# Kernel tuning notes

Hardware: AMD Instinct MI355X
Metric: run time of the kernel (lower is better)

Reference implementation:

```python
import jax, jax.numpy as jnp
import numpy as np

NUM_HEADS = 16
KV_CHANNELS = 128
MASK_FILL = -10000.0  # TE attention_mask_func fill value


def setup_inputs() -> dict:
    key = jax.random.key(0)
    k1, k2, k3 = jax.random.split(key, 3)
    S, B, H = 2048, 2, 2048
    hidden_states = jax.random.normal(k1, (S, B, H), dtype=jnp.float32)
    attention_mask = jnp.zeros((B, 1, S, S), dtype=bool)  # True = masked out
    qkv_weight = jax.random.normal(k2, (H, 3 * H), dtype=jnp.float32) * (1.0 / np.sqrt(H))
    qkv_bias = jnp.zeros((3 * H,), dtype=jnp.float32)
    proj_weight = jax.random.normal(k3, (H, H), dtype=jnp.float32) * (1.0 / np.sqrt(H))
    proj_bias = jnp.zeros((H,), dtype=jnp.float32)
    return {
        "hidden_states": hidden_states,
        "attention_mask": attention_mask,
        "qkv_weight": qkv_weight,
        "qkv_bias": qkv_bias,
        "proj_weight": proj_weight,
        "proj_bias": proj_bias,
    }


def reference(hidden_states, attention_mask, qkv_weight, qkv_bias, proj_weight, proj_bias):
    S, B, H = hidden_states.shape
    nh, d = NUM_HEADS, KV_CHANNELS
    # QKV GEMM: [s,b,H] @ [H,3H] -> [s,b,3H] -> [s,b,nh,3d] -> split
    mixed = hidden_states @ qkv_weight + qkv_bias
    mixed = mixed.reshape(S, B, nh, 3 * d)
    q, k, v = jnp.split(mixed, 3, axis=-1)  # each [s,b,nh,d]
    # BMM1 with 1/sqrt(d) scaling (layer_number=None -> no layer scaling)
    norm_factor = jnp.asarray(np.sqrt(d), dtype=hidden_states.dtype)
    scores = jnp.einsum("sbhd,tbhd->bhst", q, k) / norm_factor  # [b,nh,s,s]
    # causal mask (future positions masked) OR'd with provided bool padding mask
    causal = ~jnp.tril(jnp.ones((S, S), dtype=bool))  # True above diagonal
    mask = jnp.logical_or(causal[None, None], attention_mask)
    scores = jnp.where(mask, jnp.asarray(MASK_FILL, scores.dtype), scores)
    probs = jax.nn.softmax(scores, axis=-1)
    # dropout is identity in eval mode (training=False)
    # BMM2: [b,nh,s,t] x [t,b,nh,d] -> [s,b,nh,d] -> [s,b,H]
    context = jnp.einsum("bhst,tbhd->sbhd", probs, v).reshape(S, B, H)
    # output projection; TE Dense(use_bias=False, return_bias=True) returns bias
    out = context @ proj_weight
    return out, proj_bias
```

## Files before the change

### kernel.cpp

```cpp
#include <hip/hip_runtime.h>
#include <cstdint>
#include <math.h>

#define S_LEN 2048
#define BATCH 2
#define HID   2048
#define NHEAD 16
#define DHEAD 128

typedef _Float16 h8 __attribute__((ext_vector_type(8)));
typedef _Float16 h4 __attribute__((ext_vector_type(4)));
typedef float f32x4 __attribute__((ext_vector_type(4)));

__device__ __forceinline__ void gload16(const void* g, void* l) {
  __builtin_amdgcn_global_load_lds(
      (const __attribute__((address_space(1))) unsigned int*)g,
      (__attribute__((address_space(3))) unsigned int*)l, 16, 0, 0);
}

template <bool HAS_BIAS, bool OUT_HALF>
__global__ __launch_bounds__(512) void gemm_256v2(
    const _Float16* __restrict__ A, const _Float16* __restrict__ Bt,
    const float* __restrict__ bias, void* __restrict__ Cout, int M, int N,
    int K) {
  __shared__ _Float16 LA[2][16384];
  __shared__ _Float16 LB[2][16384];
  const int tid = (int)threadIdx.x;
  const int wave = tid >> 6, lane = tid & 63;
  const int ln = lane & 15, quad = lane >> 4;
  const int wm = wave >> 2, wn = wave & 3;
  const int bm = (int)blockIdx.y * 256, bn = (int)blockIdx.x * 256;
  const int NT = K >> 6;

  const int gc8 = ((lane & 7) ^ (lane >> 3)) * 8;
  const int rbase = wave * 8 + (lane >> 3);
  uint32_t oA[4], oB[4];
#pragma unroll
  for (int q = 0; q < 4; q++) {
    oA[q] = (uint32_t)(bm + q * 64 + rbase) * (uint32_t)K + (uint32_t)gc8;
    oB[q] = (uint32_t)(bn + q * 64 + rbase) * (uint32_t)K + (uint32_t)gc8;
  }

#define STAGEA(bb_, u_)                                                  \
  {                                                                      \
    _Pragma("unroll") for (int q = 0; q < 4; q++)                        \
        gload16(A + (oA[q] + (uint32_t)(u_)*64u),                        \
                &LA[bb_][q * 4096 + wave * 512]);                        \
  }
#define STAGEB(bb_, u_)                                                  \
  {                                                                      \
    _Pragma("unroll") for (int q = 0; q < 4; q++)                        \
        gload16(Bt + (oB[q] + (uint32_t)(u_)*64u),                       \
                &LB[bb_][q * 4096 + wave * 512]);                        \
  }

  const int arow = ln * 64;
  const int sc0 = ((quad ^ (ln & 7))) * 8;
  const int sc1 = (((4 + quad) ^ (ln & 7))) * 8;
  const int abase = wm * 8192;
  const int bbase = wn * 4096;

  f32x4 acc[8][4];
#pragma unroll
  for (int m = 0; m < 8; m++)
#pragma unroll
    for (int n = 0; n < 4; n++) acc[m][n] = (f32x4){0.f, 0.f, 0.f, 0.f};
  h8 aF[4][2], bF[4][2];

#define HALF(mo_)                                                            \
  _Pragma("unroll") for (int mm_ = 0; mm_ < 4; mm_++)                        \
      _Pragma("unroll") for (int nn_ = 0; nn_ < 4; nn_++) {                  \
    acc[(mo_) + mm_][nn_] = __builtin_amdgcn_mfma_f32_16x16x32_f16(          \
        aF[mm_][0], bF[nn_][0], acc[(mo_) + mm_][nn_], 0, 0, 0);             \
    acc[(mo_) + mm_][nn_] = __builtin_amdgcn_mfma_f32_16x16x32_f16(          \
        aF[mm_][1], bF[nn_][1], acc[(mo_) + mm_][nn_], 0, 0, 0);             \
  }

  STAGEA(0, 0) STAGEB(0, 0)
  STAGEA(1, 1) STAGEB(1, 1)
  asm volatile("s_waitcnt vmcnt(8)" ::: "memory");
  __builtin_amdgcn_s_barrier();

  for (int u = 0; u < NT; ++u) {
    const int bb = u & 1;

#pragma unroll
    for (int m = 0; m < 4; m++) {
      aF[m][0] = *(const h8*)&LA[bb][abase + m * 1024 + arow + sc0];
      aF[m][1] = *(const h8*)&LA[bb][abase + m * 1024 + arow + sc1];
    }
#pragma unroll
    for (int n = 0; n < 4; n++) {
      bF[n][0] = *(const h8*)&LB[bb][bbase + n * 1024 + arow + sc0];
      bF[n][1] = *(const h8*)&LB[bb][bbase + n * 1024 + arow + sc1];
    }
    __builtin_amdgcn_s_barrier();
    __builtin_amdgcn_s_setprio(1);
    HALF(0)
    __builtin_amdgcn_s_setprio(0);
    __builtin_amdgcn_s_barrier();

#pragma unroll
    for (int m = 0; m < 4; m++) {
      aF[m][0] = *(const h8*)&LA[bb][abase + (m + 4) * 1024 + arow + sc0];
      aF[m][1] = *(const h8*)&LA[bb][abase + (m + 4) * 1024 + arow + sc1];
    }
    if (u + 2 < NT) {
      STAGEA(bb, u + 2) STAGEB(bb, u + 2)
      asm volatile("s_waitcnt vmcnt(8)" ::: "memory");
    } else if (u + 1 < NT) {
      asm volatile("s_waitcnt vmcnt(0)" ::: "memory");
    }
    __builtin_amdgcn_s_barrier();
    __builtin_amdgcn_s_setprio(1);
    HALF(4)
    __builtin_amdgcn_s_setprio(0);
    __builtin_amdgcn_s_barrier();
  }
#undef HALF
#undef STAGEA
#undef STAGEB

#pragma unroll
  for (int m = 0; m < 8; m++) {
#pragma unroll
    for (int r = 0; r < 4; r++) {
      const size_t row = (size_t)(bm + wm * 128 + m * 16 + quad * 4 + r);
#pragma unroll
      for (int n = 0; n < 4; n++) {
        const int col = bn + wn * 64 + n * 16 + ln;
        float v = acc[m][n][r];
        if (HAS_BIAS) v += bias[col];
        if (OUT_HALF)
          ((_Float16*)Cout)[row * N + col] = (_Float16)v;
        else
          ((float*)Cout)[row * N + col] = v;
      }
    }
  }
}

template <bool HAS_BIAS, bool OUT_HALF>
__global__ __launch_bounds__(512) void gemm_128(
    const _Float16* __restrict__ A, const _Float16* __restrict__ Bt,
    const float* __restrict__ bias, void* __restrict__ Cout, int M, int N,
    int K) {
  __shared__ _Float16 LA[2][8192];
  __shared__ _Float16 LB[2][16384];
  const int tid = (int)threadIdx.x;
  const int wave = tid >> 6, lane = tid & 63;
  const int ln = lane & 15, quad = lane >> 4;
  const int wm = wave >> 2, wn = wave & 3;
  const int bm = (int)blockIdx.y * 128, bn = (int)blockIdx.x * 256;
  const int NT = K >> 6;

  const int gc8 = ((lane & 7) ^ (lane >> 3)) * 8;
  const uint32_t oA0 =
      (uint32_t)(bm + wave * 8 + (lane >> 3)) * (uint32_t)K + (uint32_t)gc8;
  const uint32_t oA1 = oA0 + (uint32_t)(64 * K);
  const uint32_t oB00 =
      (uint32_t)(bn + wave * 16 + (lane >> 3)) * (uint32_t)K + (uint32_t)gc8;
  const uint32_t oB01 = oB00 + (uint32_t)(8 * K);
  const uint32_t oB10 = oB00 + (uint32_t)(128 * K);
  const uint32_t oB11 = oB10 + (uint32_t)(8 * K);

#define STAGE128(bb_, u_)                                                    \
  {                                                                          \
    gload16(A + (oA0 + (uint32_t)(u_)*64u), &LA[bb_][wave * 512]);           \
    gload16(A + (oA1 + (uint32_t)(u_)*64u), &LA[bb_][4096 + wave * 512]);    \
    gload16(Bt + (oB00 + (uint32_t)(u_)*64u), &LB[bb_][wave * 1024]);        \
    gload16(Bt + (oB01 + (uint32_t)(u_)*64u), &LB[bb_][wave * 1024 + 512]);  \
    gload16(Bt + (oB10 + (uint32_t)(u_)*64u), &LB[bb_][8192 + wave * 1024]); \
    gload16(Bt + (oB11 + (uint32_t)(u_)*64u),                                \
            &LB[bb_][8192 + wave * 1024 + 512]);                             \
  }

  const int arow = ln * 64;
  const int sc0 = ((quad ^ (ln & 7))) * 8;
  const int sc1 = (((4 + quad) ^ (ln & 7))) * 8;
  const int abase = wm * 4096;
  const int bbase = wn * 4096;

  f32x4 acc[4][4];
#pragma unroll
  for (int m = 0; m < 4; m++)
#pragma unroll
    for (int n = 0; n < 4; n++) acc[m][n] = (f32x4){0.f, 0.f, 0.f, 0.f};
  h8 aF[4][2], bF[4][2];

#define HQUAD(n0_)                                                           \
  _Pragma("unroll") for (int mm_ = 0; mm_ < 4; mm_++)                        \
      _Pragma("unroll") for (int nn_ = 0; nn_ < 2; nn_++) {                  \
    acc[mm_][(n0_) + nn_] = __builtin_amdgcn_mfma_f32_16x16x32_f16(          \
        aF[mm_][0], bF[(n0_) + nn_][0], acc[mm_][(n0_) + nn_], 0, 0, 0);     \
    acc[mm_][(n0_) + nn_] = __builtin_amdgcn_mfma_f32_16x16x32_f16(          \
        aF[mm_][1], bF[(n0_) + nn_][1], acc[mm_][(n0_) + nn_], 0, 0, 0);     \
  }

  STAGE128(0, 0)
  STAGE128(1, 1)
  asm volatile("s_waitcnt vmcnt(6)" ::: "memory");
  __builtin_amdgcn_s_barrier();

  for (int u = 0; u < NT; ++u) {
    const int bb = u & 1;

#pragma unroll
    for (int m = 0; m < 4; m++) {
      aF[m][0] = *(const h8*)&LA[bb][abase + m * 1024 + arow + sc0];
      aF[m][1] = *(const h8*)&LA[bb][abase + m * 1024 + arow + sc1];
    }
#pragma unroll
    for (int n = 0; n < 2; n++) {
      bF[n][0] = *(const h8*)&LB[bb][bbase + n * 1024 + arow + sc0];
      bF[n][1] = *(const h8*)&LB[bb][bbase + n * 1024 + arow + sc1];
    }
    __builtin_amdgcn_s_barrier();
    __builtin_amdgcn_s_setprio(1);
    HQUAD(0)
    __builtin_amdgcn_s_setprio(0);
    __builtin_amdgcn_s_barrier();

#pragma unroll
    for (int n = 2; n < 4; n++) {
      bF[n][0] = *(const h8*)&LB[bb][bbase + n * 1024 + arow + sc0];
      bF[n][1] = *(const h8*)&LB[bb][bbase + n * 1024 + arow + sc1];
    }
    if (u + 2 < NT) {
      STAGE128(bb, u + 2)
      asm volatile("s_waitcnt vmcnt(6)" ::: "memory");
    } else if (u + 1 < NT) {
      asm volatile("s_waitcnt vmcnt(0)" ::: "memory");
    }
    __builtin_amdgcn_s_barrier();
    __builtin_amdgcn_s_setprio(1);
    HQUAD(2)
    __builtin_amdgcn_s_setprio(0);
    __builtin_amdgcn_s_barrier();
  }
#undef HQUAD
#undef STAGE128

#pragma unroll
  for (int m = 0; m < 4; m++) {
#pragma unroll
    for (int r = 0; r < 4; r++) {
      const size_t row = (size_t)(bm + wm * 64 + m * 16 + quad * 4 + r);
#pragma unroll
      for (int n = 0; n < 4; n++) {
        const int col = bn + wn * 64 + n * 16 + ln;
        float v = acc[m][n][r];
        if (HAS_BIAS) v += bias[col];
        if (OUT_HALF)
          ((_Float16*)Cout)[row * N + col] = (_Float16)v;
        else
          ((float*)Cout)[row * N + col] = v;
      }
    }
  }
}

__global__ __launch_bounds__(256) void transpose_cvt(
    const float* __restrict__ in, _Float16* __restrict__ out, int K, int N) {
  __shared__ float t[64][65];
  const int bn = blockIdx.x * 64, bk = blockIdx.y * 64;
  const int tid = (int)threadIdx.x;
  {
    const int r0 = tid >> 4, c4 = (tid & 15) * 4;
#pragma unroll
    for (int i = 0; i < 4; i++) {
      const int r = r0 + 16 * i;
      float4 v = *(const float4*)&in[(size_t)(bk + r) * N + bn + c4];
      t[r][c4] = v.x;
      t[r][c4 + 1] = v.y;
      t[r][c4 + 2] = v.z;
      t[r][c4 + 3] = v.w;
    }
  }
  __syncthreads();
  {
    const int c0 = tid >> 4, r4 = (tid & 15) * 4;
#pragma unroll
    for (int i = 0; i < 4; i++) {
      const int c = c0 + 16 * i;
      h4 o = {(_Float16)t[r4][c], (_Float16)t[r4 + 1][c],
              (_Float16)t[r4 + 2][c], (_Float16)t[r4 + 3][c]};
      *(h4*)&out[(size_t)(bn + c) * K + bk + r4] = o;
    }
  }
}

__global__ __launch_bounds__(256) void cvt_fp16(const float* __restrict__ in,
                                                _Float16* __restrict__ out,
                                                int n4) {
  int i = blockIdx.x * blockDim.x + threadIdx.x;
  if (i < n4) {
    float4 v = ((const float4*)in)[i];
    h4 o = {(_Float16)v.x, (_Float16)v.y, (_Float16)v.z, (_Float16)v.w};
    *(h4*)&out[4 * (size_t)i] = o;
  }
}

__global__ __launch_bounds__(256) void pack_mask(
    const unsigned char* __restrict__ m, uint32_t* __restrict__ pm) {
  const int i = blockIdx.x * 256 + threadIdx.x;
  const int w = i & 63, r = (i >> 6) & (S_LEN - 1), b = i >> 17;
  const uint32_t* src =
      (const uint32_t*)(m + ((size_t)b * S_LEN + r) * S_LEN + w * 32);
  uint32_t bits = 0;
#pragma unroll
  for (int k = 0; k < 8; k++) {
    const uint32_t v = src[k];
    bits |= ((v & 0x000000FFu) ? 1u : 0u) << (4 * k);
    bits |= ((v & 0x0000FF00u) ? 1u : 0u) << (4 * k + 1);
    bits |= ((v & 0x00FF0000u) ? 1u : 0u) << (4 * k + 2);
    bits |= ((v & 0xFF000000u) ? 1u : 0u) << (4 * k + 3);
  }
  const int c0 = w * 32;
  uint32_t caus;
  if (c0 > r) {
    caus = 0xFFFFFFFFu;
  } else if (r - c0 >= 31) {
    caus = 0u;
  } else {
    caus = ~((2u << (r - c0)) - 1u);
  }
  pm[i] = bits | caus;
}

__global__ __launch_bounds__(256) void pack_kv(
    const _Float16* __restrict__ mixed, _Float16* __restrict__ KP,
    _Float16* __restrict__ VP) {
  __shared__ _Float16 Tv[128 * 40];
  const int kt = blockIdx.x;
  const int z = blockIdx.y;
  const int kb = kt * 32;
  const int tid = threadIdx.x;
  const size_t RS = (size_t)BATCH * NHEAD * 384;
  const _Float16* base = mixed + (size_t)z * 384;

  {
    const int r = tid >> 3, d0 = (tid & 7) * 16;
    const _Float16* src = base + (size_t)(kb + r) * RS + 256 + d0;
    h8 v0 = *(const h8*)src;
    h8 v1 = *(const h8*)(src + 8);
#pragma unroll
    for (int e = 0; e < 8; e++) Tv[(d0 + e) * 40 + r] = v0[e];
#pragma unroll
    for (int e = 0; e < 8; e++) Tv[(d0 + 8 + e) * 40 + r] = v1[e];
  }
  __syncthreads();

  const size_t tb = ((size_t)z * 64 + kt) * 8 * 512;
#pragma unroll
  for (int c = 0; c < 2; c++) {
    const int idx = tid + 256 * c;
    const int i = idx >> 6, l = idx & 63;
    const int ln = l & 15, quad = l >> 4;
    {
      const int jn = i >> 2, kq = i & 3;
      h8 v = *(const h8*)(base + (size_t)(kb + 16 * jn + ln) * RS + 128 +
                          32 * kq + 8 * quad);
      *(h8*)&KP[tb + (size_t)i * 512 + l * 8] = v;
    }
    {
      h8 v = *(const h8*)&Tv[(16 * i + ln) * 40 + 8 * quad];
      *(h8*)&VP[tb + (size_t)i * 512 + l * 8] = v;
    }
  }
}

__global__ __launch_bounds__(512) void flash_attn_v9(
    const _Float16* __restrict__ mixed, const _Float16* __restrict__ KP,
    const _Float16* __restrict__ VP, const uint32_t* __restrict__ pmask,
    _Float16* __restrict__ ctx) {
  const int bid = (int)blockIdx.x;
  const int x = bid & 7, s = bid >> 3;
  const int z = x * 4 + (s & 3);
  const int qt = 15 - (s >> 2);
  const int h = z & (NHEAD - 1), b = z >> 4;
  const int qb = qt * 128;
  const int tid = threadIdx.x;
  const int wave = tid >> 6, lane = tid & 63;
  const int ln = lane & 15, quad = lane >> 4;

  __shared__ _Float16 Kbuf[2][8 * 512];
  __shared__ _Float16 Vbuf[2][8 * 512];
  __shared__ _Float16 St[8][16 * 40];

  const size_t RS = (size_t)BATCH * NHEAD * 384;
  const _Float16* base = mixed + (size_t)z * 384;
  const uint32_t* pmb = pmask + (size_t)b * S_LEN * 64;
  const float scale = 0.08838834764831845f;

  h8 qfrag[4];
  {
    const size_t row = (size_t)(qb + 16 * wave + ln);
#pragma unroll
    for (int kq = 0; kq < 4; kq++) {
      h8 v = *(const h8*)(base + row * RS + 32 * kq + 8 * quad);
#pragma unroll
      for (int j = 0; j < 8; j++) v[j] = (_Float16)((float)v[j] * scale);
      qfrag[kq] = v;
    }
  }

  f32x4 o[8];
#pragma unroll
  for (int nt = 0; nt < 8; nt++) o[nt] = (f32x4){0.f, 0.f, 0.f, 0.f};
  float lpart[4] = {0.f, 0.f, 0.f, 0.f};

  const int ntiles = 4 * qt + 4;

  const size_t zt = (size_t)z * 64;
#define STAGE(kt_, buf_)                                            \
  {                                                                 \
    const size_t tbk = (zt + (kt_)) * (8 * 512) + lane * 8;         \
    gload16(KP + tbk + wave * 512, &Kbuf[buf_][wave * 512]);        \
    gload16(VP + tbk + wave * 512, &Vbuf[buf_][wave * 512]);        \
  }

  STAGE(0, 0)

  const uint32_t* pmr = pmb + (size_t)(qb + 16 * wave + 4 * quad) * 64;

  for (int kt = 0; kt < ntiles; kt++) {
    const int cur = kt & 1;
    __syncthreads();

    if (kt + 1 < ntiles) STAGE(kt + 1, cur ^ 1)

    uint32_t mw[4];
#pragma unroll
    for (int r = 0; r < 4; r++) mw[r] = pmr[(size_t)r * 64 + kt];

    f32x4 sreg[2];
    sreg[0] = (f32x4){0.f, 0.f, 0.f, 0.f};
    sreg[1] = (f32x4){0.f, 0.f, 0.f, 0.f};
#pragma unroll
    for (int kq = 0; kq < 4; kq++) {
#pragma unroll
      for (int jn = 0; jn < 2; jn++) {
        h8 bk = *(const h8*)&Kbuf[cur][(jn * 4 + kq) * 512 + lane * 8];
        sreg[jn] = __builtin_amdgcn_mfma_f32_16x16x32_f16(qfrag[kq], bk,
                                                          sreg[jn], 0, 0, 0);
      }
    }

#pragma unroll
    for (int r = 0; r < 4; r++) {
      const uint32_t ms = mw[r] >> ln;
#pragma unroll
      for (int jn = 0; jn < 2; jn++) {
        const float sv =
            ((ms >> (16 * jn)) & 1u) ? -10000.0f : sreg[jn][r];
        const float p = __expf(sv);
        lpart[r] += p;
        St[wave][(4 * quad + r) * 40 + 16 * jn + ln] = (_Float16)p;
      }
    }
    __threadfence_block();

    {
      h8 ap = *(const h8*)&St[wave][ln * 40 + 8 * quad];
#pragma unroll
      for (int nt = 0; nt < 8; nt++) {
        h8 bv = *(const h8*)&Vbuf[cur][nt * 512 + lane * 8];
        o[nt] = __builtin_amdgcn_mfma_f32_16x16x32_f16(ap, bv, o[nt], 0, 0, 0);
      }
    }
  }
#undef STAGE

#pragma unroll
  for (int r = 0; r < 4; r++) {
    float l = lpart[r];
#pragma unroll
    for (int off = 8; off >= 1; off >>= 1) l += __shfl_xor(l, off, 16);
    const float inv_l = 1.0f / l;
    const size_t row_g = (size_t)(qb + 16 * wave + 4 * quad + r);
    _Float16* dst = ctx + (row_g * BATCH + b) * HID + h * DHEAD;
#pragma unroll
    for (int nt = 0; nt < 8; nt++)
      dst[16 * nt + ln] = (_Float16)(o[nt][r] * inv_l);
  }
}

__global__ void copy_bias(const float* __restrict__ src,
                          float* __restrict__ dst) {
  int i = blockIdx.x * blockDim.x + threadIdx.x;
  if (i < HID) dst[i] = src[i];
}

extern "C" void kernel_launch(void* const* d_in, const int* in_sizes, int n_in,
                              void* d_out, int out_size, void* d_ws,
                              size_t ws_size, hipStream_t stream) {
  (void)in_sizes;
  (void)n_in;
  const float* hs = (const float*)d_in[0];
  const unsigned char* mask = (const unsigned char*)d_in[1];
  const float* qkv_w = (const float*)d_in[2];
  const float* qkv_b = (const float*)d_in[3];
  const float* proj_w = (const float*)d_in[4];
  const float* proj_b = (const float*)d_in[5];
  float* out = (float*)d_out;

  const size_t M = (size_t)S_LEN * BATCH;
  const size_t mixed_e = M * 3 * HID;
  const size_t qkvwt_e = (size_t)3 * HID * HID;
  const size_t hsh_e = M * HID;
  const size_t projwt_e = (size_t)HID * HID;
  const size_t ctx_e = M * HID;
  const size_t need =
      (mixed_e + qkvwt_e + hsh_e + projwt_e + ctx_e) * sizeof(_Float16);
  if (ws_size < need) return;

  _Float16* mixed = (_Float16*)d_ws;
  _Float16* qkv_wt = mixed + mixed_e;
  _Float16* hs_h = qkv_wt + qkvwt_e;
  _Float16* proj_wt = hs_h + hsh_e;
  _Float16* ctx = proj_wt + projwt_e;
  _Float16* KP = hs_h;
  _Float16* VP = qkv_wt;
  uint32_t* pmask = (uint32_t*)out;

  cvt_fp16<<<(int)(hsh_e / 4 / 256), 256, 0, stream>>>(hs, hs_h,
                                                       (int)(hsh_e / 4));
  transpose_cvt<<<dim3(3 * HID / 64, HID / 64), 256, 0, stream>>>(
      qkv_w, qkv_wt, HID, 3 * HID);
  transpose_cvt<<<dim3(HID / 64, HID / 64), 256, 0, stream>>>(
      proj_w, proj_wt, HID, HID);
  pack_mask<<<(BATCH * S_LEN * 64) / 256, 256, 0, stream>>>(mask, pmask);

  gemm_256v2<true, true><<<dim3(16, (int)(M / 256)), 512, 0, stream>>>(
      hs_h, qkv_wt, qkv_b, mixed, (int)M, 3 * HID, HID);
  gemm_128<true, true><<<dim3(8, (int)(M / 128)), 512, 0, stream>>>(
      hs_h, qkv_wt + (size_t)4096 * HID, qkv_b + 4096,
      (void*)(mixed + 4096), (int)M, 3 * HID, HID);

  pack_kv<<<dim3(S_LEN / 32, BATCH * NHEAD), 256, 0, stream>>>(mixed, KP, VP);

  flash_attn_v9<<<512, 512, 0, stream>>>(mixed, KP, VP, pmask, ctx);

  gemm_128<false, false><<<dim3(HID / 256, M / 128), 512, 0, stream>>>(
      ctx, proj_wt, nullptr, out, (int)M, HID, HID);

  copy_bias<<<(HID + 255) / 256, 256, 0, stream>>>(proj_b, out + M * HID);
}
```

Before: 414.2 us.

## Fuse preprocessing kernels into one launch and rebalance causal attention block order

Merges the fp16 conversion, the two weight transposes, the mask packing and the bias copy into a single `prep` kernel that dispatches on block index. This removes several small launches and the gaps between them. It also remaps flash-attention block IDs: the first 256 blocks visit query tiles from heaviest to lightest, and the second 256 from lightest to heaviest. The aim is to pair long and short causal workloads and shorten the tail. The bias is now written before the attention and projection stages instead of at the end.

```diff
diff --git a/kernel.cpp b/kernel.cpp
--- a/kernel.cpp
+++ b/kernel.cpp
@@ -260,11 +260,10 @@
   }
 }
 
-__global__ __launch_bounds__(256) void transpose_cvt(
-    const float* __restrict__ in, _Float16* __restrict__ out, int K, int N) {
-  __shared__ float t[64][65];
-  const int bn = blockIdx.x * 64, bk = blockIdx.y * 64;
-  const int tid = (int)threadIdx.x;
+__device__ __forceinline__ void transpose_body(const float* in, _Float16* out,
+                                               int K, int N, int bx, int by,
+                                               int tid, float (*t)[65]) {
+  const int bn = bx * 64, bk = by * 64;
   {
     const int r0 = tid >> 4, c4 = (tid & 15) * 4;
 #pragma unroll
@@ -290,42 +289,54 @@
   }
 }
 
-__global__ __launch_bounds__(256) void cvt_fp16(const float* __restrict__ in,
-                                                _Float16* __restrict__ out,
-                                                int n4) {
-  int i = blockIdx.x * blockDim.x + threadIdx.x;
-  if (i < n4) {
-    float4 v = ((const float4*)in)[i];
+__global__ __launch_bounds__(256) void prep(
+    const float* __restrict__ hs, _Float16* __restrict__ hs_h,
+    const float* __restrict__ qkv_w, _Float16* __restrict__ qkv_wt,
+    const float* __restrict__ proj_w, _Float16* __restrict__ proj_wt,
+    const unsigned char* __restrict__ mask, uint32_t* __restrict__ pm,
+    const float* __restrict__ proj_b, float* __restrict__ bias_out) {
+  __shared__ float t[64][65];
+  const int bid = (int)blockIdx.x;
+  const int tid = (int)threadIdx.x;
+  if (bid < 8192) {
+    const int i = bid * 256 + tid;
+    float4 v = ((const float4*)hs)[i];
     h4 o = {(_Float16)v.x, (_Float16)v.y, (_Float16)v.z, (_Float16)v.w};
-    *(h4*)&out[4 * (size_t)i] = o;
-  }
-}
-
-__global__ __launch_bounds__(256) void pack_mask(
-    const unsigned char* __restrict__ m, uint32_t* __restrict__ pm) {
-  const int i = blockIdx.x * 256 + threadIdx.x;
-  const int w = i & 63, r = (i >> 6) & (S_LEN - 1), b = i >> 17;
-  const uint32_t* src =
-      (const uint32_t*)(m + ((size_t)b * S_LEN + r) * S_LEN + w * 32);
-  uint32_t bits = 0;
-#pragma unroll
-  for (int k = 0; k < 8; k++) {
-    const uint32_t v = src[k];
-    bits |= ((v & 0x000000FFu) ? 1u : 0u) << (4 * k);
-    bits |= ((v & 0x0000FF00u) ? 1u : 0u) << (4 * k + 1);
-    bits |= ((v & 0x00FF0000u) ? 1u : 0u) << (4 * k + 2);
-    bits |= ((v & 0xFF000000u) ? 1u : 0u) << (4 * k + 3);
-  }
-  const int c0 = w * 32;
-  uint32_t caus;
-  if (c0 > r) {
-    caus = 0xFFFFFFFFu;
-  } else if (r - c0 >= 31) {
-    caus = 0u;
+    *(h4*)&hs_h[4 * (size_t)i] = o;
+  } else if (bid < 11264) {
+    const int r = bid - 8192;
+    transpose_body(qkv_w, qkv_wt, HID, 3 * HID, r % 96, r / 96, tid, t);
+  } else if (bid < 12288) {
+    const int r = bid - 11264;
+    transpose_body(proj_w, proj_wt, HID, HID, r % 32, r / 32, tid, t);
+  } else if (bid < 13312) {
+    const int i = (bid - 12288) * 256 + tid;
+    const int w = i & 63, rr = (i >> 6) & (S_LEN - 1), b = i >> 17;
+    const uint32_t* src =
+        (const uint32_t*)(mask + ((size_t)b * S_LEN + rr) * S_LEN + w * 32);
+    uint32_t bits = 0;
+#pragma unroll
+    for (int k = 0; k < 8; k++) {
+      const uint32_t v = src[k];
+      bits |= ((v & 0x000000FFu) ? 1u : 0u) << (4 * k);
+      bits |= ((v & 0x0000FF00u) ? 1u : 0u) << (4 * k + 1);
+      bits |= ((v & 0x00FF0000u) ? 1u : 0u) << (4 * k + 2);
+      bits |= ((v & 0xFF000000u) ? 1u : 0u) << (4 * k + 3);
+    }
+    const int c0 = w * 32;
+    uint32_t caus;
+    if (c0 > rr) {
+      caus = 0xFFFFFFFFu;
+    } else if (rr - c0 >= 31) {
+      caus = 0u;
+    } else {
+      caus = ~((2u << (rr - c0)) - 1u);
+    }
+    pm[i] = bits | caus;
   } else {
-    caus = ~((2u << (r - c0)) - 1u);
-  }
-  pm[i] = bits | caus;
+    const int i = (bid - 13312) * 256 + tid;
+    if (i < HID) bias_out[i] = proj_b[i];
+  }
 }
 
 __global__ __launch_bounds__(256) void pack_kv(
@@ -370,14 +381,15 @@
   }
 }
 
-__global__ __launch_bounds__(512) void flash_attn_v9(
+__global__ __launch_bounds__(512) void flash_attn_v11(
     const _Float16* __restrict__ mixed, const _Float16* __restrict__ KP,
     const _Float16* __restrict__ VP, const uint32_t* __restrict__ pmask,
     _Float16* __restrict__ ctx) {
   const int bid = (int)blockIdx.x;
-  const int x = bid & 7, s = bid >> 3;
-  const int z = x * 4 + (s & 3);
-  const int qt = 15 - (s >> 2);
+  const int u = bid & 255, hi = bid >> 8;
+  const int qi = u >> 5;
+  const int z = (u & 7) * 4 + ((u >> 3) & 3);
+  const int qt = hi ? qi : 15 - qi;
   const int h = z & (NHEAD - 1), b = z >> 4;
   const int qb = qt * 128;
   const int tid = threadIdx.x;
@@ -484,12 +496,6 @@
     for (int nt = 0; nt < 8; nt++)
       dst[16 * nt + ln] = (_Float16)(o[nt][r] * inv_l);
   }
-}
-
-__global__ void copy_bias(const float* __restrict__ src,
-                          float* __restrict__ dst) {
-  int i = blockIdx.x * blockDim.x + threadIdx.x;
-  if (i < HID) dst[i] = src[i];
 }
 
 extern "C" void kernel_launch(void* const* d_in, const int* in_sizes, int n_in,
@@ -524,13 +530,8 @@
   _Float16* VP = qkv_wt;
   uint32_t* pmask = (uint32_t*)out;
 
-  cvt_fp16<<<(int)(hsh_e / 4 / 256), 256, 0, stream>>>(hs, hs_h,
-                                                       (int)(hsh_e / 4));
-  transpose_cvt<<<dim3(3 * HID / 64, HID / 64), 256, 0, stream>>>(
-      qkv_w, qkv_wt, HID, 3 * HID);
-  transpose_cvt<<<dim3(HID / 64, HID / 64), 256, 0, stream>>>(
-      proj_w, proj_wt, HID, HID);
-  pack_mask<<<(BATCH * S_LEN * 64) / 256, 256, 0, stream>>>(mask, pmask);
+  prep<<<13320, 256, 0, stream>>>(hs, hs_h, qkv_w, qkv_wt, proj_w, proj_wt,
+                                  mask, pmask, proj_b, out + M * HID);
 
   gemm_256v2<true, true><<<dim3(16, (int)(M / 256)), 512, 0, stream>>>(
       hs_h, qkv_wt, qkv_b, mixed, (int)M, 3 * HID, HID);
@@ -540,10 +541,8 @@
 
   pack_kv<<<dim3(S_LEN / 32, BATCH * NHEAD), 256, 0, stream>>>(mixed, KP, VP);
 
-  flash_attn_v9<<<512, 512, 0, stream>>>(mixed, KP, VP, pmask, ctx);
+  flash_attn_v11<<<512, 512, 0, stream>>>(mixed, KP, VP, pmask, ctx);
 
   gemm_128<false, false><<<dim3(HID / 256, M / 128), 512, 0, stream>>>(
       ctx, proj_wt, nullptr, out, (int)M, HID, HID);
-
-  copy_bias<<<(HID + 255) / 256, 256, 0, stream>>>(proj_b, out + M * HID);
-}
+}
```

After: 404.1 us. -2.4%, faster.
